# Kernel tuning notes

Hardware: AMD Instinct MI355X
Metric: run time of the kernel (lower is better)

The kernel has to match this reference:

```python
import jax, jax.numpy as jnp
import numpy as np


def _conv1x1(x, w, b):
    # x: (B,C_in,H,W), w: (C_out,C_in), b: (C_out,)
    return jnp.einsum('bchw,oc->bohw', x, w) + b[None, :, None, None]


def _maxpool2x2(x):
    B, C, H, W = x.shape
    return x.reshape(B, C, H // 2, 2, W // 2, 2).max(axis=(3, 5))


def setup_inputs() -> dict:
    key = jax.random.key(0)
    ks = jax.random.split(key, 10)
    B, C, H, W = 16, 64, 64, 64
    d8, d2 = C // 8, C // 2
    s = 0.05
    return {
        'x': jax.random.normal(ks[0], (B, C, H, W), dtype=jnp.float32),
        'w_theta': jax.random.normal(ks[1], (d8, C), dtype=jnp.float32) * s,
        'b_theta': jnp.zeros((d8,), dtype=jnp.float32),
        'w_phi': jax.random.normal(ks[2], (d8, C), dtype=jnp.float32) * s,
        'b_phi': jnp.zeros((d8,), dtype=jnp.float32),
        'w_g': jax.random.normal(ks[3], (d2, C), dtype=jnp.float32) * s,
        'b_g': jnp.zeros((d2,), dtype=jnp.float32),
        'w_o': jax.random.normal(ks[4], (C, d2), dtype=jnp.float32) * s,
        'b_o': jnp.zeros((C,), dtype=jnp.float32),
        'sigma': jnp.ones((1,), dtype=jnp.float32),
    }


def reference(x, w_theta, b_theta, w_phi, b_phi, w_g, b_g, w_o, b_o, sigma):
    B, C, H, W = x.shape
    N = H * W
    theta = _conv1x1(x, w_theta, b_theta).reshape(B, C // 8, N)            # (B, d8, N)
    phi = _maxpool2x2(_conv1x1(x, w_phi, b_phi)).reshape(B, C // 8, N // 4)  # (B, d8, N/4)
    attn = jax.nn.softmax(jnp.einsum('bdn,bdm->bnm', theta, phi), axis=-1)   # (B, N, N/4)
    g = _maxpool2x2(_conv1x1(x, w_g, b_g)).reshape(B, C // 2, N // 4)        # (B, d2, N/4)
    attn_g = jnp.einsum('bcm,bnm->bcn', g, attn).reshape(B, C // 2, H, W)
    attn_g = _conv1x1(attn_g, w_o, b_o)
    return x + sigma[0] * attn_g
```

## Files before the change

### kernel.cpp

```cpp
#include <hip/hip_runtime.h>


#define B_   16
#define C_   64
#define HW_  4096
#define M_   1024

typedef __attribute__((ext_vector_type(8))) short bf16x8;
typedef __attribute__((ext_vector_type(4))) float f32x4;
typedef __attribute__((ext_vector_type(4))) _Float16 f16x4;

#define LOG2E 1.44269504088896340736f

__device__ __forceinline__ unsigned short f2bf(float f) {
    union { float f; unsigned int u; } v; v.f = f;
    return (unsigned short)((v.u + 0x7FFFu + ((v.u >> 16) & 1u)) >> 16);
}
__device__ __forceinline__ unsigned int packh2(float a, float b) {
    auto h = __builtin_amdgcn_cvt_pkrtz(a, b);
    union { decltype(h) h; unsigned int u; } v;
    v.h = h;
    return v.u;
}
__device__ __forceinline__ unsigned int pack2t(float a, float b) {
    union { float f; unsigned int u; } ua, ub; ua.f = a; ub.f = b;
    return (ua.u >> 16) | (ub.u & 0xFFFF0000u);
}

__global__ __launch_bounds__(256) void proj_kernel(
    const float* __restrict__ x,
    const float* __restrict__ w_theta, const float* __restrict__ b_theta,
    const float* __restrict__ w_phi,   const float* __restrict__ b_phi,
    const float* __restrict__ w_g,     const float* __restrict__ b_g,
    unsigned short* __restrict__ thetaH,
    unsigned short* __restrict__ phiH,
    unsigned short* __restrict__ gTp)
{
    __shared__ __align__(16) float x_l[64 * 132];
    __shared__ float pool_l[128][41];

    const int tid = threadIdx.x;
    const int b   = blockIdx.y;
    const int rp  = blockIdx.x;
    const int n0  = rp * 128;

    {
        const float4* src = (const float4*)(x + (size_t)b * C_ * HW_ + n0);
        #pragma unroll
        for (int j = 0; j < 8; j++) {
            int idx = tid + j * 256;
            int c = idx >> 5, p4 = idx & 31;
            float4 v = src[(size_t)c * (HW_ / 4) + p4];
            *(float4*)&x_l[c * 132 + p4 * 4] = v;
        }
    }
    __syncthreads();

    const int px = tid & 127;
    const int og = tid >> 7;

    if (og == 0) {
        float th[8], ph[8], g0[8];
        #pragma unroll
        for (int o = 0; o < 8; o++) { th[o] = b_theta[o]; ph[o] = b_phi[o]; g0[o] = b_g[o]; }
        #pragma unroll 4
        for (int c = 0; c < C_; c++) {
            float xv = x_l[c * 132 + px];
            #pragma unroll
            for (int o = 0; o < 8; o++) th[o] += xv * w_theta[o * 64 + c];
            #pragma unroll
            for (int o = 0; o < 8; o++) ph[o] += xv * w_phi[o * 64 + c];
            #pragma unroll
            for (int o = 0; o < 8; o++) g0[o] += xv * w_g[o * 64 + c];
        }
        unsigned short* tout = thetaH + ((size_t)b * HW_ + n0 + px) * 8;
        uint4 tv;
        tv.x = packh2(th[0] * LOG2E, th[1] * LOG2E);
        tv.y = packh2(th[2] * LOG2E, th[3] * LOG2E);
        tv.z = packh2(th[4] * LOG2E, th[5] * LOG2E);
        tv.w = packh2(th[6] * LOG2E, th[7] * LOG2E);
        *(uint4*)tout = tv;
        #pragma unroll
        for (int o = 0; o < 8; o++) { pool_l[px][o] = ph[o]; pool_l[px][8 + o] = g0[o]; }
    } else {
        float gg[24];
        #pragma unroll
        for (int o = 0; o < 24; o++) gg[o] = b_g[8 + o];
        #pragma unroll 4
        for (int c = 0; c < C_; c++) {
            float xv = x_l[c * 132 + px];
            #pragma unroll
            for (int o = 0; o < 24; o++) gg[o] += xv * w_g[(8 + o) * 64 + c];
        }
        #pragma unroll
        for (int o = 0; o < 24; o++) pool_l[px][16 + o] = gg[o];
    }
    __syncthreads();

    {
        const int j   = tid & 31;
        const int grp = tid >> 5;
        const int p00 = 2 * j, p01 = 2 * j + 1, p10 = 64 + 2 * j, p11 = 65 + 2 * j;
        const int mq   = rp * 32 + j;
        const int pcol = rp * 32 + ((j >> 2) & 3) * 8 + (j >> 4) * 4 + (j & 3);
        #pragma unroll
        for (int k = 0; k < 5; k++) {
            const int ch = grp * 5 + k;
            float v = fmaxf(fmaxf(pool_l[p00][ch], pool_l[p01][ch]),
                            fmaxf(pool_l[p10][ch], pool_l[p11][ch]));
            if (ch < 8)
                ((_Float16*)phiH)[((size_t)b * M_ + mq) * 16 + ch] = (_Float16)v;
            else
                gTp[((size_t)b * 32 + (ch - 8)) * M_ + pcol] = f2bf(v);
        }
        if (tid < 32) {
            *(uint4*)((_Float16*)phiH + ((size_t)b * M_ + rp * 32 + tid) * 16 + 8) =
                make_uint4(0, 0, 0, 0);
        }
    }
}

__global__ __launch_bounds__(256, 4) void attn_kernel(
    const float* __restrict__ x,
    const unsigned short* __restrict__ thetaH,
    const unsigned short* __restrict__ phiH,
    const unsigned short* __restrict__ gTp,
    const float* __restrict__ w_o, const float* __restrict__ b_o,
    const float* __restrict__ sigma,
    float* __restrict__ out)
{
    __shared__ float Op_l[4][64 * 33];
    __shared__ float rs_l[4][64];

    const int tid   = threadIdx.x;
    const int b     = blockIdx.y;
    const int qbase = blockIdx.x * 64;
    const int wv    = tid >> 6;
    const int lane  = tid & 63;
    const int ln15  = lane & 15;
    const int quad  = lane >> 4;

    const _Float16* phiP = (const _Float16*)phiH + (size_t)b * M_ * 16;
    const unsigned short* gP = gTp + (size_t)b * 32 * M_;

    f16x4 th[4];
    {
        const f16x4 z = {0, 0, 0, 0};
        #pragma unroll
        for (int qt = 0; qt < 4; qt++) {
            const _Float16* tp = (const _Float16*)thetaH
                + ((size_t)b * HW_ + qbase + qt * 16 + ln15) * 8 + (quad & 1) * 4;
            f16x4 t = *(const f16x4*)tp;
            th[qt] = (quad < 2) ? t : z;
        }
    }

    #define LD_PHI(ch_, mt_) \
        (*(const f16x4*)(phiP + ((ch_) * 64 + (mt_) * 16 + ln15) * 16 + quad * 4))
    #define LD_G(ch_, h_, s_) \
        (*(const bf16x8*)(gP + (size_t)((h_) * 16 + ln15) * M_ + (ch_) * 64 + (s_) * 32 + quad * 8))

    f32x4 acc[2][4];
    #pragma unroll
    for (int h = 0; h < 2; h++)
        #pragma unroll
        for (int qt = 0; qt < 4; qt++) acc[h][qt] = (f32x4){0.f, 0.f, 0.f, 0.f};
    float rs_p[4] = {0.f, 0.f, 0.f, 0.f};

    #pragma unroll
    for (int wc = 0; wc < 4; wc++) {
        const int ch = wv * 4 + wc;
        f16x4 pf[4];
        #pragma unroll
        for (int mt = 0; mt < 4; mt++) pf[mt] = LD_PHI(ch, mt);
        bf16x8 gf[2][2];
        gf[0][0] = LD_G(ch, 0, 0); gf[0][1] = LD_G(ch, 0, 1);
        gf[1][0] = LD_G(ch, 1, 0); gf[1][1] = LD_G(ch, 1, 1);

        #pragma unroll
        for (int s = 0; s < 2; s++) {
            #pragma unroll
            for (int qt = 0; qt < 4; qt++) {
                const f32x4 zc = {0.f, 0.f, 0.f, 0.f};
                f32x4 S0 = __builtin_amdgcn_mfma_f32_16x16x16f16(pf[2 * s],     th[qt], zc, 0, 0, 0);
                f32x4 S1 = __builtin_amdgcn_mfma_f32_16x16x16f16(pf[2 * s + 1], th[qt], zc, 0, 0, 0);
                float e0[4], e1[4];
                #pragma unroll
                for (int r = 0; r < 4; r++) {
                    e0[r] = exp2f(S0[r]);
                    e1[r] = exp2f(S1[r]);
                    rs_p[qt] += e0[r] + e1[r];
                }
                union { bf16x8 v; unsigned int u[4]; } pb;
                pb.u[0] = pack2t(e0[0], e0[1]); pb.u[1] = pack2t(e0[2], e0[3]);
                pb.u[2] = pack2t(e1[0], e1[1]); pb.u[3] = pack2t(e1[2], e1[3]);
                acc[0][qt] = __builtin_amdgcn_mfma_f32_16x16x32_bf16(gf[0][s], pb.v, acc[0][qt], 0, 0, 0);
                acc[1][qt] = __builtin_amdgcn_mfma_f32_16x16x32_bf16(gf[1][s], pb.v, acc[1][qt], 0, 0, 0);
            }
        }
    }
    #undef LD_PHI
    #undef LD_G

    {
        float v[4];
        #pragma unroll
        for (int qt = 0; qt < 4; qt++) {
            float t = rs_p[qt];
            t += __shfl_xor(t, 16);
            t += __shfl_xor(t, 32);
            v[qt] = t;
        }
        if (quad == 0) {
            #pragma unroll
            for (int qt = 0; qt < 4; qt++) rs_l[wv][qt * 16 + ln15] = v[qt];
        }
    }
    #pragma unroll
    for (int h = 0; h < 2; h++)
        #pragma unroll
        for (int qt = 0; qt < 4; qt++)
            #pragma unroll
            for (int r = 0; r < 4; r++)
                Op_l[wv][(qt * 16 + ln15) * 33 + h * 16 + quad * 4 + r] = acc[h][qt][r];
    __syncthreads();

    const int q = tid & 63;
    const float rowsum = rs_l[0][q] + rs_l[1][q] + rs_l[2][q] + rs_l[3][q];
    const float sg  = sigma[0];
    const float inv = sg / rowsum;
    float o[32];
    #pragma unroll
    for (int c = 0; c < 32; c++)
        o[c] = Op_l[0][q * 33 + c] + Op_l[1][q * 33 + c]
             + Op_l[2][q * 33 + c] + Op_l[3][q * 33 + c];
    const size_t xb = (size_t)b * C_ * HW_ + qbase + q;
    #pragma unroll
    for (int k = 0; k < 16; k++) {
        const int co = wv * 16 + k;
        float t = 0.f;
        #pragma unroll
        for (int c = 0; c < 32; c++) t += w_o[co * 32 + c] * o[c];
        out[xb + (size_t)co * HW_] = x[xb + (size_t)co * HW_] + t * inv + sg * b_o[co];
    }
}

extern "C" void kernel_launch(void* const* d_in, const int* in_sizes, int n_in,
                              void* d_out, int out_size, void* d_ws, size_t ws_size,
                              hipStream_t stream)
{
    const float* x       = (const float*)d_in[0];
    const float* w_theta = (const float*)d_in[1];
    const float* b_theta = (const float*)d_in[2];
    const float* w_phi   = (const float*)d_in[3];
    const float* b_phi   = (const float*)d_in[4];
    const float* w_g     = (const float*)d_in[5];
    const float* b_g     = (const float*)d_in[6];
    const float* w_o     = (const float*)d_in[7];
    const float* b_o     = (const float*)d_in[8];
    const float* sigma   = (const float*)d_in[9];
    float* out = (float*)d_out;

    unsigned short* thetaH = (unsigned short*)d_ws;
    unsigned short* phiH   = thetaH + (size_t)B_ * HW_ * 8;
    unsigned short* gTp    = phiH   + (size_t)B_ * M_ * 16;

    proj_kernel<<<dim3(32, B_), 256, 0, stream>>>(
        x, w_theta, b_theta, w_phi, b_phi, w_g, b_g, thetaH, phiH, gTp);
    attn_kernel<<<dim3(64, B_), 256, 0, stream>>>(
        x, thetaH, phiH, gTp, w_o, b_o, sigma, out);
}
```

Baseline: 129.2 us.

## Give each wave its own 16 queries and apply the output projection with MFMA

The attention kernel previously split the key dimension across the four waves, with every wave covering all 64 queries, and reduced the partial outputs and row sums through shared memory plus a block barrier. Now each wave owns 16 queries and walks all 16 key chunks itself, double-buffering the phi and g fragment loads for the next chunk. This removes the LDS reduction and the __syncthreads. The final 32-to-64 output 1x1 conv becomes bf16 MFMAs using a w_o copy that proj_kernel pre-converts and permutes, replacing the scalar FMA loop. This costs extra bf16 rounding of the attention output and each wave re-reading the full phi and g per batch.

```diff
diff --git a/kernel.cpp b/kernel.cpp
--- a/kernel.cpp
+++ b/kernel.cpp
@@ -32,9 +32,11 @@
     const float* __restrict__ w_theta, const float* __restrict__ b_theta,
     const float* __restrict__ w_phi,   const float* __restrict__ b_phi,
     const float* __restrict__ w_g,     const float* __restrict__ b_g,
+    const float* __restrict__ w_o,
     unsigned short* __restrict__ thetaH,
     unsigned short* __restrict__ phiH,
-    unsigned short* __restrict__ gTp)
+    unsigned short* __restrict__ gTp,
+    unsigned short* __restrict__ w_oB)
 {
     __shared__ __align__(16) float x_l[64 * 132];
     __shared__ float pool_l[128][41];
@@ -118,6 +120,18 @@
                 make_uint4(0, 0, 0, 0);
         }
     }
+
+    if (rp == 0 && b == 0) {
+        #pragma unroll
+        for (int i = 0; i < 8; i++) {
+            const int e   = tid * 8 + i;
+            const int k   = e & 31;
+            const int row = (e >> 5) & 15;
+            const int cot = e >> 9;
+            const int c   = ((k >> 2) & 1) * 16 + ((k >> 3) << 2) + (k & 3);
+            w_oB[e] = f2bf(w_o[(cot * 16 + row) * 32 + c]);
+        }
+    }
 }
 
 __global__ __launch_bounds__(256, 4) void attn_kernel(
@@ -125,34 +139,29 @@
     const unsigned short* __restrict__ thetaH,
     const unsigned short* __restrict__ phiH,
     const unsigned short* __restrict__ gTp,
-    const float* __restrict__ w_o, const float* __restrict__ b_o,
+    const unsigned short* __restrict__ w_oB,
+    const float* __restrict__ b_o,
     const float* __restrict__ sigma,
     float* __restrict__ out)
 {
-    __shared__ float Op_l[4][64 * 33];
-    __shared__ float rs_l[4][64];
-
     const int tid   = threadIdx.x;
     const int b     = blockIdx.y;
-    const int qbase = blockIdx.x * 64;
     const int wv    = tid >> 6;
     const int lane  = tid & 63;
     const int ln15  = lane & 15;
     const int quad  = lane >> 4;
+    const int wq    = blockIdx.x * 64 + wv * 16;
 
     const _Float16* phiP = (const _Float16*)phiH + (size_t)b * M_ * 16;
     const unsigned short* gP = gTp + (size_t)b * 32 * M_;
 
-    f16x4 th[4];
+    f16x4 th;
     {
+        const _Float16* tp = (const _Float16*)thetaH
+            + ((size_t)b * HW_ + wq + ln15) * 8 + (quad & 1) * 4;
+        f16x4 t = *(const f16x4*)tp;
         const f16x4 z = {0, 0, 0, 0};
-        #pragma unroll
-        for (int qt = 0; qt < 4; qt++) {
-            const _Float16* tp = (const _Float16*)thetaH
-                + ((size_t)b * HW_ + qbase + qt * 16 + ln15) * 8 + (quad & 1) * 4;
-            f16x4 t = *(const f16x4*)tp;
-            th[qt] = (quad < 2) ? t : z;
-        }
+        th = (quad < 2) ? t : z;
     }
 
     #define LD_PHI(ch_, mt_) \
@@ -160,88 +169,77 @@
     #define LD_G(ch_, h_, s_) \
         (*(const bf16x8*)(gP + (size_t)((h_) * 16 + ln15) * M_ + (ch_) * 64 + (s_) * 32 + quad * 8))
 
-    f32x4 acc[2][4];
-    #pragma unroll
-    for (int h = 0; h < 2; h++)
-        #pragma unroll
-        for (int qt = 0; qt < 4; qt++) acc[h][qt] = (f32x4){0.f, 0.f, 0.f, 0.f};
-    float rs_p[4] = {0.f, 0.f, 0.f, 0.f};
-
-    #pragma unroll
-    for (int wc = 0; wc < 4; wc++) {
-        const int ch = wv * 4 + wc;
-        f16x4 pf[4];
-        #pragma unroll
-        for (int mt = 0; mt < 4; mt++) pf[mt] = LD_PHI(ch, mt);
-        bf16x8 gf[2][2];
-        gf[0][0] = LD_G(ch, 0, 0); gf[0][1] = LD_G(ch, 0, 1);
-        gf[1][0] = LD_G(ch, 1, 0); gf[1][1] = LD_G(ch, 1, 1);
-
+    f32x4 acc0 = {0.f, 0.f, 0.f, 0.f};
+    f32x4 acc1 = {0.f, 0.f, 0.f, 0.f};
+    float rs_p = 0.f;
+
+    f16x4  pf[2][4];
+    bf16x8 gf[2][4];
+
+    #pragma unroll
+    for (int mt = 0; mt < 4; mt++) pf[0][mt] = LD_PHI(0, mt);
+    gf[0][0] = LD_G(0, 0, 0); gf[0][1] = LD_G(0, 0, 1);
+    gf[0][2] = LD_G(0, 1, 0); gf[0][3] = LD_G(0, 1, 1);
+
+    #pragma unroll
+    for (int ch = 0; ch < 16; ch++) {
+        const int cur = ch & 1, nxt = cur ^ 1;
+        if (ch < 15) {
+            #pragma unroll
+            for (int mt = 0; mt < 4; mt++) pf[nxt][mt] = LD_PHI(ch + 1, mt);
+            gf[nxt][0] = LD_G(ch + 1, 0, 0); gf[nxt][1] = LD_G(ch + 1, 0, 1);
+            gf[nxt][2] = LD_G(ch + 1, 1, 0); gf[nxt][3] = LD_G(ch + 1, 1, 1);
+        }
         #pragma unroll
         for (int s = 0; s < 2; s++) {
-            #pragma unroll
-            for (int qt = 0; qt < 4; qt++) {
-                const f32x4 zc = {0.f, 0.f, 0.f, 0.f};
-                f32x4 S0 = __builtin_amdgcn_mfma_f32_16x16x16f16(pf[2 * s],     th[qt], zc, 0, 0, 0);
-                f32x4 S1 = __builtin_amdgcn_mfma_f32_16x16x16f16(pf[2 * s + 1], th[qt], zc, 0, 0, 0);
-                float e0[4], e1[4];
-                #pragma unroll
-                for (int r = 0; r < 4; r++) {
-                    e0[r] = exp2f(S0[r]);
-                    e1[r] = exp2f(S1[r]);
-                    rs_p[qt] += e0[r] + e1[r];
-                }
-                union { bf16x8 v; unsigned int u[4]; } pb;
-                pb.u[0] = pack2t(e0[0], e0[1]); pb.u[1] = pack2t(e0[2], e0[3]);
-                pb.u[2] = pack2t(e1[0], e1[1]); pb.u[3] = pack2t(e1[2], e1[3]);
-                acc[0][qt] = __builtin_amdgcn_mfma_f32_16x16x32_bf16(gf[0][s], pb.v, acc[0][qt], 0, 0, 0);
-                acc[1][qt] = __builtin_amdgcn_mfma_f32_16x16x32_bf16(gf[1][s], pb.v, acc[1][qt], 0, 0, 0);
+            const f32x4 zc = {0.f, 0.f, 0.f, 0.f};
+            f32x4 S0 = __builtin_amdgcn_mfma_f32_16x16x16f16(pf[cur][2 * s],     th, zc, 0, 0, 0);
+            f32x4 S1 = __builtin_amdgcn_mfma_f32_16x16x16f16(pf[cur][2 * s + 1], th, zc, 0, 0, 0);
+            float e0[4], e1[4];
+            #pragma unroll
+            for (int r = 0; r < 4; r++) {
+                e0[r] = exp2f(S0[r]);
+                e1[r] = exp2f(S1[r]);
+                rs_p += e0[r] + e1[r];
             }
+            union { bf16x8 v; unsigned int u[4]; } pb;
+            pb.u[0] = pack2t(e0[0], e0[1]); pb.u[1] = pack2t(e0[2], e0[3]);
+            pb.u[2] = pack2t(e1[0], e1[1]); pb.u[3] = pack2t(e1[2], e1[3]);
+            acc0 = __builtin_amdgcn_mfma_f32_16x16x32_bf16(gf[cur][s],     pb.v, acc0, 0, 0, 0);
+            acc1 = __builtin_amdgcn_mfma_f32_16x16x32_bf16(gf[cur][2 + s], pb.v, acc1, 0, 0, 0);
         }
     }
     #undef LD_PHI
     #undef LD_G
 
-    {
-        float v[4];
-        #pragma unroll
-        for (int qt = 0; qt < 4; qt++) {
-            float t = rs_p[qt];
-            t += __shfl_xor(t, 16);
-            t += __shfl_xor(t, 32);
-            v[qt] = t;
-        }
-        if (quad == 0) {
-            #pragma unroll
-            for (int qt = 0; qt < 4; qt++) rs_l[wv][qt * 16 + ln15] = v[qt];
-        }
-    }
-    #pragma unroll
-    for (int h = 0; h < 2; h++)
-        #pragma unroll
-        for (int qt = 0; qt < 4; qt++)
-            #pragma unroll
-            for (int r = 0; r < 4; r++)
-                Op_l[wv][(qt * 16 + ln15) * 33 + h * 16 + quad * 4 + r] = acc[h][qt][r];
-    __syncthreads();
-
-    const int q = tid & 63;
-    const float rowsum = rs_l[0][q] + rs_l[1][q] + rs_l[2][q] + rs_l[3][q];
+    bf16x8 wf[4];
+    #pragma unroll
+    for (int t4 = 0; t4 < 4; t4++)
+        wf[t4] = *(const bf16x8*)(w_oB + t4 * 512 + ln15 * 32 + quad * 8);
+
+    float rs = rs_p;
+    rs += __shfl_xor(rs, 16);
+    rs += __shfl_xor(rs, 32);
     const float sg  = sigma[0];
-    const float inv = sg / rowsum;
-    float o[32];
-    #pragma unroll
-    for (int c = 0; c < 32; c++)
-        o[c] = Op_l[0][q * 33 + c] + Op_l[1][q * 33 + c]
-             + Op_l[2][q * 33 + c] + Op_l[3][q * 33 + c];
-    const size_t xb = (size_t)b * C_ * HW_ + qbase + q;
-    #pragma unroll
-    for (int k = 0; k < 16; k++) {
-        const int co = wv * 16 + k;
-        float t = 0.f;
-        #pragma unroll
-        for (int c = 0; c < 32; c++) t += w_o[co * 32 + c] * o[c];
-        out[xb + (size_t)co * HW_] = x[xb + (size_t)co * HW_] + t * inv + sg * b_o[co];
+    const float inv = sg / rs;
+
+    union { bf16x8 v; unsigned int u[4]; } ob;
+    ob.u[0] = pack2t(acc0[0] * inv, acc0[1] * inv);
+    ob.u[1] = pack2t(acc0[2] * inv, acc0[3] * inv);
+    ob.u[2] = pack2t(acc1[0] * inv, acc1[1] * inv);
+    ob.u[3] = pack2t(acc1[2] * inv, acc1[3] * inv);
+
+    const f32x4 zc = {0.f, 0.f, 0.f, 0.f};
+    const size_t xq = (size_t)b * C_ * HW_ + wq + ln15;
+    #pragma unroll
+    for (int t4 = 0; t4 < 4; t4++) {
+        f32x4 oo = __builtin_amdgcn_mfma_f32_16x16x32_bf16(wf[t4], ob.v, zc, 0, 0, 0);
+        #pragma unroll
+        for (int r = 0; r < 4; r++) {
+            const int co = t4 * 16 + quad * 4 + r;
+            const size_t idx = xq + (size_t)co * HW_;
+            out[idx] = x[idx] + oo[r] + sg * b_o[co];
+        }
     }
 }
 
@@ -264,9 +262,10 @@
     unsigned short* thetaH = (unsigned short*)d_ws;
     unsigned short* phiH   = thetaH + (size_t)B_ * HW_ * 8;
     unsigned short* gTp    = phiH   + (size_t)B_ * M_ * 16;
+    unsigned short* w_oB   = gTp    + (size_t)B_ * 32 * M_;
 
     proj_kernel<<<dim3(32, B_), 256, 0, stream>>>(
-        x, w_theta, b_theta, w_phi, b_phi, w_g, b_g, thetaH, phiH, gTp);
+        x, w_theta, b_theta, w_phi, b_phi, w_g, b_g, w_o, thetaH, phiH, gTp, w_oB);
     attn_kernel<<<dim3(64, B_), 256, 0, stream>>>(
-        x, thetaH, phiH, gTp, w_o, b_o, sigma, out);
-}
+        x, thetaH, phiH, gTp, w_oB, b_o, sigma, out);
+}
```

Result: slower. 165.4 us (+28.1%).
